# Kernel optimization log

Measured on AMD Instinct MI355X. Metric: run time of the kernel, lower is better.

The kernel has to match this reference:

```python
import jax, jax.numpy as jnp
import numpy as np

B, S, H, I, E, K = 2, 1024, 768, 1536, 8, 2
CAPACITY_FACTOR = 1.5
ROUTING_TEMP = 1.0
LB_WEIGHT = 0.001


def setup_inputs() -> dict:
    key = jax.random.key(0)
    k_x, k_g, k_w1, k_w3, k_w2 = jax.random.split(key, 5)
    std = 0.02
    return {
        "x": jax.random.normal(k_x, (B, S, H), dtype=jnp.float32),
        "w_gate": jax.random.normal(k_g, (H, E), dtype=jnp.float32) * 0.02,
        "w1": jax.random.normal(k_w1, (E, H, I), dtype=jnp.float32) * std,
        "w3": jax.random.normal(k_w3, (E, H, I), dtype=jnp.float32) * std,
        "w2": jax.random.normal(k_w2, (E, I, H), dtype=jnp.float32) * (std / np.sqrt(2 * 12)),
    }


def _moe_forward(x, w_gate, w1, w3, w2):
    Bb, Ss, Hh = x.shape
    T = Bb * Ss
    xf = x.reshape(T, Hh)

    # --- routing ---
    gate_logits = (xf @ w_gate) / ROUTING_TEMP          # [T, E]
    gate_probs = jax.nn.softmax(gate_logits, axis=-1)   # [T, E]
    topk_probs, topk_idx = jax.lax.top_k(gate_probs, K)  # [T, K]
    topk_probs = topk_probs / (topk_probs.sum(-1, keepdims=True) + 1e-8)

    # --- capacity dropping (per-k slot, token order, like the torch loop) ---
    capacity = max(8, int((T * K // E) * CAPACITY_FACTOR))
    onehot = (topk_idx[:, :, None] == jnp.arange(E)[None, None, :])  # [T, K, E] bool
    ranks = jnp.cumsum(onehot.astype(jnp.int32), axis=0)             # position of token in expert queue
    keep = onehot & (ranks <= capacity)                               # [T, K, E]

    # combine weight per (token, expert): sum over k of kept, clamped routing prob
    w_clamped = jnp.clip(topk_probs, 1e-8, 10.0)                      # [T, K]
    combine = jnp.einsum("tk,tke->te", w_clamped, keep.astype(xf.dtype))  # [T, E]

    # --- dense per-expert SwiGLU (reference form of masked dispatch) ---
    g = jnp.einsum("th,ehi->tei", xf, w1)   # [T, E, I]
    u = jnp.einsum("th,ehi->tei", xf, w3)   # [T, E, I]
    h = jax.nn.silu(g) * u                    # [T, E, I]
    y = jnp.einsum("tei,eih->teh", h, w2)   # [T, E, H]
    out = jnp.einsum("te,teh->th", combine, y).reshape(Bb, Ss, Hh)

    # --- load balancing loss ---
    expert_counts = keep.sum(axis=(0, 1)).astype(jnp.float32)         # [E]
    dropped = (onehot.sum() - keep.sum()).astype(jnp.float32)
    expert_usage = jax.lax.stop_gradient(expert_counts) / float(max(T * K, 1))
    gate_importance = gate_probs.mean(axis=0)                          # [E]
    aux = jnp.sum(expert_usage * gate_importance) * E
    aux = aux + jnp.where(dropped > 0, dropped / float(max(T, 1)) * 0.1, 0.0)
    aux = jnp.minimum(aux, 1.0) * LB_WEIGHT
    return out, aux


def reference(x, w_gate, w1, w3, w2):
    return _moe_forward(x, w_gate, w1, w3, w2)
```

## Files before the change

kernel.cpp:

```cpp
#include <hip/hip_runtime.h>
#include <math.h>

#define T_TOK 2048
#define HD 768
#define ID 1536
#define NE 8
#define CAP 768
#define TK 4096
#define RT 12
#define NB1 24
#define KC1 24
#define NB2 12
#define KC2 48
#define W2BLK 576

typedef __bf16 bf16_t;
typedef __bf16 bf16x8 __attribute__((ext_vector_type(8)));
typedef __bf16 bf16x4 __attribute__((ext_vector_type(4)));
typedef float floatx4 __attribute__((ext_vector_type(4)));

__device__ __forceinline__ void gld16(const bf16_t* g, bf16_t* l) {
  __builtin_amdgcn_global_load_lds(
      (__attribute__((address_space(1))) void*)(g),
      (__attribute__((address_space(3))) void*)(l),
      16, 0, 0);
}

__device__ __forceinline__ void repack_unit256(const float* __restrict__ src,
                                               bf16_t* __restrict__ dst, int C,
                                               int kc0, int tid) {
  int n = tid >> 2, p4 = tid & 3;
  int c8 = p4 ^ ((n >> 1) & 3);
  const float* sp0 = src + n + (size_t)(kc0 * 32 + c8 * 8) * C;
  bf16_t* dp = dst + (size_t)kc0 * 2048 + tid * 8;
#pragma unroll 2
  for (int t = 0; t < 8; ++t) {
    const float* sp = sp0 + (size_t)t * 32 * C;
    float v[8];
#pragma unroll
    for (int j = 0; j < 8; ++j) v[j] = sp[(size_t)j * C];
    bf16x8 o;
#pragma unroll
    for (int j = 0; j < 8; ++j) o[j] = (bf16_t)v[j];
    *(bf16x8*)(dp + t * 2048) = o;
  }
}

__device__ __forceinline__ void repack_unit1024(const float* __restrict__ src,
                                                bf16_t* __restrict__ dst, int C,
                                                int kc0, int tid1024) {
  int tid = tid1024 & 255;
  int tq = tid1024 >> 8;
  int n = tid >> 2, p4 = tid & 3;
  int c8 = p4 ^ ((n >> 1) & 3);
  const float* sp0 = src + n + (size_t)(kc0 * 32 + c8 * 8) * C;
  bf16_t* dp = dst + (size_t)kc0 * 2048 + tid * 8;
#pragma unroll
  for (int tt = 0; tt < 2; ++tt) {
    int t = tq * 2 + tt;
    const float* sp = sp0 + (size_t)t * 32 * C;
    float v[8];
#pragma unroll
    for (int j = 0; j < 8; ++j) v[j] = sp[(size_t)j * C];
    bf16x8 o;
#pragma unroll
    for (int j = 0; j < 8; ++j) o[j] = (bf16_t)v[j];
    *(bf16x8*)(dp + t * 2048) = o;
  }
}

__global__ void k_route(const float* __restrict__ x, const float* __restrict__ wg,
                        bf16_t* __restrict__ xbf, int2* __restrict__ idx2,
                        float2* __restrict__ wc2, float* __restrict__ probs8) {
  int b = blockIdx.x;
  int tid = threadIdx.x;
  int t = b * 4 + (tid >> 6);
  int lane = tid & 63;
  const float* xr = x + (size_t)t * HD;
  int off = lane * 12;
  float4 a = *(const float4*)(xr + off);
  float4 bv = *(const float4*)(xr + off + 4);
  float4 c = *(const float4*)(xr + off + 8);
  float xv[12] = {a.x, a.y, a.z, a.w, bv.x, bv.y, bv.z, bv.w, c.x, c.y, c.z, c.w};
  bf16x4 s0, s1, s2;
#pragma unroll
  for (int j = 0; j < 4; ++j) { s0[j] = (bf16_t)xv[j]; s1[j] = (bf16_t)xv[4 + j]; s2[j] = (bf16_t)xv[8 + j]; }
  bf16_t* xo = xbf + (size_t)t * HD + off;
  *(bf16x4*)xo = s0; *(bf16x4*)(xo + 4) = s1; *(bf16x4*)(xo + 8) = s2;

  float acc[8] = {0, 0, 0, 0, 0, 0, 0, 0};
#pragma unroll
  for (int jj = 0; jj < 12; ++jj) {
    const float4* wr = (const float4*)(wg + (size_t)(off + jj) * 8);
    float4 w0 = wr[0], w1v = wr[1];
    float v = xv[jj];
    acc[0] += v * w0.x; acc[1] += v * w0.y; acc[2] += v * w0.z; acc[3] += v * w0.w;
    acc[4] += v * w1v.x; acc[5] += v * w1v.y; acc[6] += v * w1v.z; acc[7] += v * w1v.w;
  }
#pragma unroll
  for (int e = 0; e < 8; ++e) {
    float v = acc[e];
    for (int s = 1; s < 64; s <<= 1) v += __shfl_xor(v, s, 64);
    acc[e] = v;
  }
  float mx = acc[0];
#pragma unroll
  for (int e = 1; e < 8; ++e) mx = fmaxf(mx, acc[e]);
  float p[8], sum = 0.f;
#pragma unroll
  for (int e = 0; e < 8; ++e) { p[e] = __expf(acc[e] - mx); sum += p[e]; }
#pragma unroll
  for (int e = 0; e < 8; ++e) p[e] /= sum;
  if (lane == 0) {
    float4 P0 = make_float4(p[0], p[1], p[2], p[3]);
    float4 P1 = make_float4(p[4], p[5], p[6], p[7]);
    *(float4*)&probs8[t * 8] = P0;
    *(float4*)&probs8[t * 8 + 4] = P1;
    int e0 = 0;
#pragma unroll
    for (int e = 1; e < 8; ++e) if (p[e] > p[e0]) e0 = e;
    int e1 = (e0 == 0) ? 1 : 0;
#pragma unroll
    for (int e = 0; e < 8; ++e) if (e != e0 && p[e] > p[e1]) e1 = e;
    float denom = p[e0] + p[e1] + 1e-8f;
    float w0c = fminf(fmaxf(p[e0] / denom, 1e-8f), 10.f);
    float w1c = fminf(fmaxf(p[e1] / denom, 1e-8f), 10.f);
    idx2[t] = make_int2(e0, e1);
    wc2[t] = make_float2(w0c, w1c);
  }
}

__global__ void k_scan(const int2* __restrict__ idx2, const float2* __restrict__ wc2,
                       const float* __restrict__ probs8,
                       const float* __restrict__ w1, const float* __restrict__ w3,
                       bf16_t* __restrict__ w1b, bf16_t* __restrict__ w3b,
                       int* __restrict__ tok_of_row, int2* __restrict__ rows2,
                       int2* __restrict__ cnt_start, float* __restrict__ aux_out) {
  if (blockIdx.x > 0) {
    int rb = blockIdx.x - 1;
    int m = rb >= 576;
    int r3 = m ? rb - 576 : rb;
    int pan = r3 / 3;
    int kc0 = (r3 - pan * 3) * 8;
    int e = pan & 7, nb = pan >> 3;
    const float* src = (m ? w3 : w1) + (size_t)e * HD * ID + nb * 64;
    bf16_t* dst = (m ? w3b : w1b) + (size_t)(e * NB1 + nb) * (KC1 * 2048);
    repack_unit1024(src, dst, ID, kc0, threadIdx.x);
    return;
  }
  __shared__ int2 sIdx[2048];
  __shared__ int sTot[16];
  __shared__ int sPos[8];
  __shared__ float sImp[16][8];
  int tid = threadIdx.x;
  sIdx[tid] = idx2[tid]; sIdx[tid + 1024] = idx2[tid + 1024];
  rows2[tid] = make_int2(-1, -1); rows2[tid + 1024] = make_int2(-1, -1);
  const float4* pp = (const float4*)probs8;
  float4 u0 = pp[tid * 4], u1 = pp[tid * 4 + 1], u2 = pp[tid * 4 + 2], u3 = pp[tid * 4 + 3];
  float im[8] = {u0.x + u2.x, u0.y + u2.y, u0.z + u2.z, u0.w + u2.w,
                 u1.x + u3.x, u1.y + u3.y, u1.z + u3.z, u1.w + u3.w};
#pragma unroll
  for (int e = 0; e < 8; ++e) {
    float v = im[e];
    for (int d = 1; d < 64; d <<= 1) v += __shfl_xor(v, d, 64);
    im[e] = v;
  }
  int w = tid >> 6, lane = tid & 63;
  if (lane == 0) {
#pragma unroll
    for (int e = 0; e < 8; ++e) sImp[w][e] = im[e];
  }
  __syncthreads();
  int s = w >> 3, e = w & 7;
  int t0 = lane * 32;
  int cnt = 0;
  for (int j = 0; j < 32; ++j) {
    int2 p = sIdx[t0 + j];
    cnt += ((s ? p.y : p.x) == e) ? 1 : 0;
  }
  int incl = cnt;
  for (int d = 1; d < 64; d <<= 1) {
    int v = __shfl_up(incl, d, 64);
    if (lane >= d) incl += v;
  }
  int excl = incl - cnt;
  if (lane == 63) sTot[w] = incl;
  __syncthreads();
  if (tid == 0) {
    int run = 0; float a = 0.f;
    for (int ee = 0; ee < 8; ++ee) {
      float impv = 0.f;
      for (int ww = 0; ww < 16; ++ww) impv += sImp[ww][ee];
      int k = min(sTot[ee], CAP) + min(sTot[8 + ee], CAP);
      sPos[ee] = run;
      cnt_start[ee] = make_int2(run, k);
      a += ((float)k / (float)TK) * (impv / (float)T_TOK);
      run += k;
    }
    a *= (float)NE;
    int dropped = TK - run;
    if (dropped > 0) a += (float)dropped / (float)T_TOK * 0.1f;
    aux_out[0] = fminf(a, 1.f) * 0.001f;
  }
  __syncthreads();
  int rank = excl;
  for (int j = 0; j < 32; ++j) {
    int t = t0 + j;
    int2 p = sIdx[t];
    int ex = s ? p.y : p.x;
    if (ex == e) {
      rank++;
      if (rank <= CAP) {
        int pos = atomicAdd(&sPos[e], 1);
        tok_of_row[pos] = t;
        ((int*)rows2)[2 * t + s] = pos;
      }
    }
  }
}

__global__ __launch_bounds__(256, 4)
void k_gemm1(const bf16_t* __restrict__ xbf, const bf16_t* __restrict__ w1b,
             const bf16_t* __restrict__ w3b, const float* __restrict__ w2,
             bf16_t* __restrict__ w2b, const int* __restrict__ tok_of_row,
             const int2* __restrict__ cnt_start, bf16_t* __restrict__ h_ws) {
  if (blockIdx.x < W2BLK) {
    int q = blockIdx.x;
    int pan = q / 6;
    int kc0 = (q - pan * 6) * 8;
    int e = pan & 7, nb = pan >> 3;
    const float* src = w2 + (size_t)e * ID * HD + nb * 64;
    bf16_t* dst = w2b + (size_t)(e * NB2 + nb) * (KC2 * 2048);
    repack_unit256(src, dst, HD, kc0, threadIdx.x);
    return;
  }
  int bx = blockIdx.x - W2BLK;
  int e = bx & 7;
  int t = bx >> 3;
  int nb = t / RT, rt = t - nb * RT;
  int2 cs = cnt_start[e];
  int nrows = cs.y - rt * 128;
  if (nrows <= 0) return;
  if (nrows > 128) nrows = 128;
  int grow0 = cs.x + rt * 128;

  __shared__ __attribute__((aligned(16))) bf16_t Abuf[2][128 * 32];
  __shared__ __attribute__((aligned(16))) bf16_t B1buf[2][64 * 32];
  __shared__ __attribute__((aligned(16))) bf16_t B3buf[2][64 * 32];

  int tid = threadIdx.x;
  int lane = tid & 63, wv = tid >> 6;
  int wm = wv & 1, wn = wv >> 1;
  int lr = lane & 15, q = lane >> 4;
  int rdc = (q ^ ((lane >> 1) & 3)) * 8;
  int srow = lane >> 2;
  int gch = ((lane & 3) ^ ((lane >> 3) & 3)) * 8;

  int ra = wv * 32 + srow;
  int tokA0 = tok_of_row[grow0 + min(ra, nrows - 1)];
  int tokA1 = tok_of_row[grow0 + min(ra + 16, nrows - 1)];
  const bf16_t* gA0 = xbf + (size_t)tokA0 * HD + gch;
  const bf16_t* gA1 = xbf + (size_t)tokA1 * HD + gch;
  const bf16_t* p1 = w1b + (size_t)((e * NB1 + nb) * KC1) * 2048 + tid * 8;
  const bf16_t* p3 = w3b + (size_t)((e * NB1 + nb) * KC1) * 2048 + tid * 8;

  floatx4 accg[4][2] = {};
  floatx4 accu[4][2] = {};

  gld16(gA0, &Abuf[0][wv * 1024]); gld16(gA1, &Abuf[0][wv * 1024 + 512]);
  gld16(p1, &B1buf[0][wv * 512]); gld16(p3, &B3buf[0][wv * 512]);
  gA0 += 32; gA1 += 32; p1 += 2048; p3 += 2048;
  __syncthreads();

  for (int kk = 0; kk < KC1; ++kk) {
    int cur = kk & 1;
    if (kk + 1 < KC1) {
      int nxt = cur ^ 1;
      gld16(gA0, &Abuf[nxt][wv * 1024]); gld16(gA1, &Abuf[nxt][wv * 1024 + 512]);
      gld16(p1, &B1buf[nxt][wv * 512]); gld16(p3, &B3buf[nxt][wv * 512]);
      gA0 += 32; gA1 += 32; p1 += 2048; p3 += 2048;
    }
    bf16x8 af[4], b1f[2], b3f[2];
#pragma unroll
    for (int i = 0; i < 4; ++i) af[i] = *(const bf16x8*)&Abuf[cur][(wm * 64 + i * 16 + lr) * 32 + rdc];
#pragma unroll
    for (int i = 0; i < 2; ++i) b1f[i] = *(const bf16x8*)&B1buf[cur][(wn * 32 + i * 16 + lr) * 32 + rdc];
#pragma unroll
    for (int i = 0; i < 2; ++i) b3f[i] = *(const bf16x8*)&B3buf[cur][(wn * 32 + i * 16 + lr) * 32 + rdc];
#pragma unroll
    for (int i = 0; i < 4; ++i)
#pragma unroll
      for (int jj = 0; jj < 2; ++jj) {
        accg[i][jj] = __builtin_amdgcn_mfma_f32_16x16x32_bf16(af[i], b1f[jj], accg[i][jj], 0, 0, 0);
        accu[i][jj] = __builtin_amdgcn_mfma_f32_16x16x32_bf16(af[i], b3f[jj], accu[i][jj], 0, 0, 0);
      }
    if (kk + 1 < KC1) __syncthreads();
  }
#pragma unroll
  for (int i = 0; i < 4; ++i)
#pragma unroll
    for (int r = 0; r < 4; ++r) {
      int rl = wm * 64 + i * 16 + q * 4 + r;
      if (rl < nrows) {
        size_t rb = (size_t)(grow0 + rl) * ID + nb * 64 + wn * 32 + lr;
#pragma unroll
        for (int jj = 0; jj < 2; ++jj) {
          float gg = accg[i][jj][r], uu = accu[i][jj][r];
          float sg = gg / (1.f + __expf(-gg));
          h_ws[rb + jj * 16] = (bf16_t)(sg * uu);
        }
      }
    }
}

__global__ __launch_bounds__(256, 4)
void k_gemm2(const bf16_t* __restrict__ h_ws, const bf16_t* __restrict__ w2b,
             const int2* __restrict__ cnt_start, float* __restrict__ y) {
  int e = blockIdx.x & 7;
  int t = blockIdx.x >> 3;
  int nb = t / RT, rt = t - nb * RT;
  int2 cs = cnt_start[e];
  int nrows = cs.y - rt * 128;
  if (nrows <= 0) return;
  if (nrows > 128) nrows = 128;
  int grow0 = cs.x + rt * 128;

  __shared__ __attribute__((aligned(16))) bf16_t Abuf[2][128 * 32];
  __shared__ __attribute__((aligned(16))) bf16_t Bbuf[2][64 * 32];

  int tid = threadIdx.x;
  int lane = tid & 63, wv = tid >> 6;
  int wm = wv & 1, wn = wv >> 1;
  int lr = lane & 15, q = lane >> 4;
  int rdc = (q ^ ((lane >> 1) & 3)) * 8;
  int srow = lane >> 2;
  int gch = ((lane & 3) ^ ((lane >> 3) & 3)) * 8;

  int ra = wv * 32 + srow;
  const bf16_t* gA0 = h_ws + (size_t)(grow0 + min(ra, nrows - 1)) * ID + gch;
  const bf16_t* gA1 = h_ws + (size_t)(grow0 + min(ra + 16, nrows - 1)) * ID + gch;
  const bf16_t* pB = w2b + (size_t)((e * NB2 + nb) * KC2) * 2048 + tid * 8;

  floatx4 acc[4][2] = {};

  gld16(gA0, &Abuf[0][wv * 1024]); gld16(gA1, &Abuf[0][wv * 1024 + 512]);
  gld16(pB, &Bbuf[0][wv * 512]);
  gA0 += 32; gA1 += 32; pB += 2048;
  __syncthreads();

  for (int kk = 0; kk < KC2; ++kk) {
    int cur = kk & 1;
    if (kk + 1 < KC2) {
      int nxt = cur ^ 1;
      gld16(gA0, &Abuf[nxt][wv * 1024]); gld16(gA1, &Abuf[nxt][wv * 1024 + 512]);
      gld16(pB, &Bbuf[nxt][wv * 512]);
      gA0 += 32; gA1 += 32; pB += 2048;
    }
    bf16x8 af[4], bfr[2];
#pragma unroll
    for (int i = 0; i < 4; ++i) af[i] = *(const bf16x8*)&Abuf[cur][(wm * 64 + i * 16 + lr) * 32 + rdc];
#pragma unroll
    for (int i = 0; i < 2; ++i) bfr[i] = *(const bf16x8*)&Bbuf[cur][(wn * 32 + i * 16 + lr) * 32 + rdc];
#pragma unroll
    for (int i = 0; i < 4; ++i)
#pragma unroll
      for (int jj = 0; jj < 2; ++jj)
        acc[i][jj] = __builtin_amdgcn_mfma_f32_16x16x32_bf16(af[i], bfr[jj], acc[i][jj], 0, 0, 0);
    if (kk + 1 < KC2) __syncthreads();
  }
#pragma unroll
  for (int i = 0; i < 4; ++i)
#pragma unroll
    for (int r = 0; r < 4; ++r) {
      int rl = wm * 64 + i * 16 + q * 4 + r;
      if (rl < nrows) {
        size_t ob = (size_t)(grow0 + rl) * HD + nb * 64 + wn * 32 + lr;
#pragma unroll
        for (int jj = 0; jj < 2; ++jj)
          y[ob + jj * 16] = acc[i][jj][r];
      }
    }
}

__global__ void k_comb(const float* __restrict__ y, const int2* __restrict__ rows2,
                       const float2* __restrict__ wc2, float* __restrict__ out) {
  int tid = threadIdx.x;
  int t = blockIdx.x * 4 + (tid >> 6);
  int lane = tid & 63;
  int2 r = rows2[t];
  float2 w = wc2[t];
  int off = lane * 12;
  floatx4 o0 = {0.f, 0.f, 0.f, 0.f}, o1 = o0, o2 = o0;
  if (r.x >= 0) {
    const float* yr = y + (size_t)r.x * HD + off;
    floatx4 a = *(const floatx4*)(yr);
    floatx4 b = *(const floatx4*)(yr + 4);
    floatx4 c = *(const floatx4*)(yr + 8);
    o0 += w.x * a; o1 += w.x * b; o2 += w.x * c;
  }
  if (r.y >= 0) {
    const float* yr = y + (size_t)r.y * HD + off;
    floatx4 a = *(const floatx4*)(yr);
    floatx4 b = *(const floatx4*)(yr + 4);
    floatx4 c = *(const floatx4*)(yr + 8);
    o0 += w.y * a; o1 += w.y * b; o2 += w.y * c;
  }
  float* op = out + (size_t)t * HD + off;
  *(floatx4*)(op) = o0;
  *(floatx4*)(op + 4) = o1;
  *(floatx4*)(op + 8) = o2;
}

extern "C" void kernel_launch(void* const* d_in, const int* in_sizes, int n_in,
                              void* d_out, int out_size, void* d_ws, size_t ws_size,
                              hipStream_t stream) {
  const float* x  = (const float*)d_in[0];
  const float* wg = (const float*)d_in[1];
  const float* w1 = (const float*)d_in[2];
  const float* w3 = (const float*)d_in[3];
  const float* w2 = (const float*)d_in[4];
  float* out = (float*)d_out;

  char* ws = (char*)d_ws;
  bf16_t* xbf  = (bf16_t*)(ws + 0);
  bf16_t* w1b  = (bf16_t*)(ws + 3145728);
  bf16_t* w3b  = (bf16_t*)(ws + 22020096);
  bf16_t* w2b  = (bf16_t*)(ws + 40894464);
  bf16_t* h_ws = (bf16_t*)(ws + 59768832);
  float*  probs8     = (float*)(ws + 72351744);
  int2*   idx2       = (int2*)(ws + 72417280);
  float2* wc2        = (float2*)(ws + 72433664);
  int*    tok_of_row = (int*)(ws + 72450048);
  int2*   rows2      = (int2*)(ws + 72466432);
  int2*   cnt_start  = (int2*)(ws + 72482816);
  float*  y_ws = (float*)(ws + 3145728);

  float* aux_out = out + (size_t)T_TOK * HD;

  k_route<<<512, 256, 0, stream>>>(x, wg, xbf, idx2, wc2, probs8);
  k_scan<<<1 + 1152, 1024, 0, stream>>>(idx2, wc2, probs8, w1, w3, w1b, w3b,
                                        tok_of_row, rows2, cnt_start, aux_out);
  k_gemm1<<<W2BLK + 8 * NB1 * RT, 256, 0, stream>>>(xbf, w1b, w3b, w2, w2b,
                                                    tok_of_row, cnt_start, h_ws);
  k_gemm2<<<8 * NB2 * RT, 256, 0, stream>>>(h_ws, w2b, cnt_start, y_ws);
  k_comb<<<512, 256, 0, stream>>>(y_ws, rows2, wc2, out);
}
```

Measured before the change: 238.4 us.

## Deepen LDS pipelining in expert GEMMs to triple and quad buffering

Both expert GEMM kernels move from double-buffered to deeper multi-stage LDS pipelines, three stages for the gate/up GEMM and four for the down GEMM. They use explicit vmcnt waits with raw s_barrier instead of __syncthreads, so several tiles' global-to-LDS loads stay in flight. The aim is to hide global load latency behind MFMA work. The cost is more shared memory per block, which may lower occupancy under the launch bounds, and the hand-counted vmcnt values must match the exact number of outstanding loads.

```diff
diff --git a/kernel.cpp b/kernel.cpp
--- a/kernel.cpp
+++ b/kernel.cpp
@@ -244,9 +244,9 @@
   if (nrows > 128) nrows = 128;
   int grow0 = cs.x + rt * 128;
 
-  __shared__ __attribute__((aligned(16))) bf16_t Abuf[2][128 * 32];
-  __shared__ __attribute__((aligned(16))) bf16_t B1buf[2][64 * 32];
-  __shared__ __attribute__((aligned(16))) bf16_t B3buf[2][64 * 32];
+  __shared__ __attribute__((aligned(16))) bf16_t Abuf[3][128 * 32];
+  __shared__ __attribute__((aligned(16))) bf16_t B1buf[3][64 * 32];
+  __shared__ __attribute__((aligned(16))) bf16_t B3buf[3][64 * 32];
 
   int tid = threadIdx.x;
   int lane = tid & 63, wv = tid >> 6;
@@ -267,19 +267,24 @@
   floatx4 accg[4][2] = {};
   floatx4 accu[4][2] = {};
 
-  gld16(gA0, &Abuf[0][wv * 1024]); gld16(gA1, &Abuf[0][wv * 1024 + 512]);
-  gld16(p1, &B1buf[0][wv * 512]); gld16(p3, &B3buf[0][wv * 512]);
-  gA0 += 32; gA1 += 32; p1 += 2048; p3 += 2048;
-  __syncthreads();
+#define STAGE1(j)                                                        \
+  do {                                                                   \
+    int s_ = (j) % 3;                                                    \
+    gld16(gA0 + (size_t)(j) * 32, &Abuf[s_][wv * 1024]);                 \
+    gld16(gA1 + (size_t)(j) * 32, &Abuf[s_][wv * 1024 + 512]);           \
+    gld16(p1 + (size_t)(j) * 2048, &B1buf[s_][wv * 512]);                \
+    gld16(p3 + (size_t)(j) * 2048, &B3buf[s_][wv * 512]);                \
+  } while (0)
+
+  STAGE1(0);
+  STAGE1(1);
+  asm volatile("s_waitcnt vmcnt(4)" ::: "memory");
+  __builtin_amdgcn_s_barrier();
+  __builtin_amdgcn_sched_barrier(0);
 
   for (int kk = 0; kk < KC1; ++kk) {
-    int cur = kk & 1;
-    if (kk + 1 < KC1) {
-      int nxt = cur ^ 1;
-      gld16(gA0, &Abuf[nxt][wv * 1024]); gld16(gA1, &Abuf[nxt][wv * 1024 + 512]);
-      gld16(p1, &B1buf[nxt][wv * 512]); gld16(p3, &B3buf[nxt][wv * 512]);
-      gA0 += 32; gA1 += 32; p1 += 2048; p3 += 2048;
-    }
+    int cur = kk % 3;
+    if (kk + 2 < KC1) STAGE1(kk + 2);
     bf16x8 af[4], b1f[2], b3f[2];
 #pragma unroll
     for (int i = 0; i < 4; ++i) af[i] = *(const bf16x8*)&Abuf[cur][(wm * 64 + i * 16 + lr) * 32 + rdc];
@@ -294,8 +299,18 @@
         accg[i][jj] = __builtin_amdgcn_mfma_f32_16x16x32_bf16(af[i], b1f[jj], accg[i][jj], 0, 0, 0);
         accu[i][jj] = __builtin_amdgcn_mfma_f32_16x16x32_bf16(af[i], b3f[jj], accu[i][jj], 0, 0, 0);
       }
-    if (kk + 1 < KC1) __syncthreads();
-  }
+    __builtin_amdgcn_sched_barrier(0);
+    if (kk + 1 < KC1) {
+      if (kk + 2 < KC1) {
+        asm volatile("s_waitcnt vmcnt(4)" ::: "memory");
+      } else {
+        asm volatile("s_waitcnt vmcnt(0)" ::: "memory");
+      }
+      __builtin_amdgcn_s_barrier();
+      __builtin_amdgcn_sched_barrier(0);
+    }
+  }
+#undef STAGE1
 #pragma unroll
   for (int i = 0; i < 4; ++i)
 #pragma unroll
@@ -325,8 +340,8 @@
   if (nrows > 128) nrows = 128;
   int grow0 = cs.x + rt * 128;
 
-  __shared__ __attribute__((aligned(16))) bf16_t Abuf[2][128 * 32];
-  __shared__ __attribute__((aligned(16))) bf16_t Bbuf[2][64 * 32];
+  __shared__ __attribute__((aligned(16))) bf16_t Abuf[4][128 * 32];
+  __shared__ __attribute__((aligned(16))) bf16_t Bbuf[4][64 * 32];
 
   int tid = threadIdx.x;
   int lane = tid & 63, wv = tid >> 6;
@@ -343,19 +358,24 @@
 
   floatx4 acc[4][2] = {};
 
-  gld16(gA0, &Abuf[0][wv * 1024]); gld16(gA1, &Abuf[0][wv * 1024 + 512]);
-  gld16(pB, &Bbuf[0][wv * 512]);
-  gA0 += 32; gA1 += 32; pB += 2048;
-  __syncthreads();
+#define STAGE2(j)                                                        \
+  do {                                                                   \
+    int s_ = (j) & 3;                                                    \
+    gld16(gA0 + (size_t)(j) * 32, &Abuf[s_][wv * 1024]);                 \
+    gld16(gA1 + (size_t)(j) * 32, &Abuf[s_][wv * 1024 + 512]);           \
+    gld16(pB + (size_t)(j) * 2048, &Bbuf[s_][wv * 512]);                 \
+  } while (0)
+
+  STAGE2(0);
+  STAGE2(1);
+  STAGE2(2);
+  asm volatile("s_waitcnt vmcnt(6)" ::: "memory");
+  __builtin_amdgcn_s_barrier();
+  __builtin_amdgcn_sched_barrier(0);
 
   for (int kk = 0; kk < KC2; ++kk) {
-    int cur = kk & 1;
-    if (kk + 1 < KC2) {
-      int nxt = cur ^ 1;
-      gld16(gA0, &Abuf[nxt][wv * 1024]); gld16(gA1, &Abuf[nxt][wv * 1024 + 512]);
-      gld16(pB, &Bbuf[nxt][wv * 512]);
-      gA0 += 32; gA1 += 32; pB += 2048;
-    }
+    int cur = kk & 3;
+    if (kk + 3 < KC2) STAGE2(kk + 3);
     bf16x8 af[4], bfr[2];
 #pragma unroll
     for (int i = 0; i < 4; ++i) af[i] = *(const bf16x8*)&Abuf[cur][(wm * 64 + i * 16 + lr) * 32 + rdc];
@@ -366,8 +386,20 @@
 #pragma unroll
       for (int jj = 0; jj < 2; ++jj)
         acc[i][jj] = __builtin_amdgcn_mfma_f32_16x16x32_bf16(af[i], bfr[jj], acc[i][jj], 0, 0, 0);
-    if (kk + 1 < KC2) __syncthreads();
-  }
+    __builtin_amdgcn_sched_barrier(0);
+    if (kk + 1 < KC2) {
+      if (kk + 3 < KC2) {
+        asm volatile("s_waitcnt vmcnt(6)" ::: "memory");
+      } else if (kk + 2 < KC2) {
+        asm volatile("s_waitcnt vmcnt(3)" ::: "memory");
+      } else {
+        asm volatile("s_waitcnt vmcnt(0)" ::: "memory");
+      }
+      __builtin_amdgcn_s_barrier();
+      __builtin_amdgcn_sched_barrier(0);
+    }
+  }
+#undef STAGE2
 #pragma unroll
   for (int i = 0; i < 4; ++i)
 #pragma unroll
```

Result: slower. 248.0 us (+4.0%).

## Widen gemm1 N tile to 128 and drop LDS double buffering

Applied to the files above, without the earlier changes.

The gate/up GEMM tile grows from 128x64 to 128x128 output columns per block, so each block reuses its gathered A rows across twice as many columns and the grid halves. The LDS buffers become single-buffered, with a sync before and after each load stage, and occupancy hints drop to 2 blocks per CU to make room for the doubled accumulators. This cuts redundant A-gather traffic, but load latency is no longer overlapped with MFMA work inside a block and fewer blocks are resident.

```diff
diff --git a/kernel.cpp b/kernel.cpp
--- a/kernel.cpp
+++ b/kernel.cpp
@@ -9,6 +9,7 @@
 #define TK 4096
 #define RT 12
 #define NB1 24
+#define NB1X 12
 #define KC1 24
 #define NB2 12
 #define KC2 48
@@ -219,7 +220,7 @@
   }
 }
 
-__global__ __launch_bounds__(256, 4)
+__global__ __launch_bounds__(256, 2)
 void k_gemm1(const bf16_t* __restrict__ xbf, const bf16_t* __restrict__ w1b,
              const bf16_t* __restrict__ w3b, const float* __restrict__ w2,
              bf16_t* __restrict__ w2b, const int* __restrict__ tok_of_row,
@@ -244,9 +245,9 @@
   if (nrows > 128) nrows = 128;
   int grow0 = cs.x + rt * 128;
 
-  __shared__ __attribute__((aligned(16))) bf16_t Abuf[2][128 * 32];
-  __shared__ __attribute__((aligned(16))) bf16_t B1buf[2][64 * 32];
-  __shared__ __attribute__((aligned(16))) bf16_t B3buf[2][64 * 32];
+  __shared__ __attribute__((aligned(16))) bf16_t Abuf[128 * 32];
+  __shared__ __attribute__((aligned(16))) bf16_t B1buf[128 * 32];
+  __shared__ __attribute__((aligned(16))) bf16_t B3buf[128 * 32];
 
   int tid = threadIdx.x;
   int lane = tid & 63, wv = tid >> 6;
@@ -261,40 +262,39 @@
   int tokA1 = tok_of_row[grow0 + min(ra + 16, nrows - 1)];
   const bf16_t* gA0 = xbf + (size_t)tokA0 * HD + gch;
   const bf16_t* gA1 = xbf + (size_t)tokA1 * HD + gch;
-  const bf16_t* p1 = w1b + (size_t)((e * NB1 + nb) * KC1) * 2048 + tid * 8;
-  const bf16_t* p3 = w3b + (size_t)((e * NB1 + nb) * KC1) * 2048 + tid * 8;
-
-  floatx4 accg[4][2] = {};
-  floatx4 accu[4][2] = {};
-
-  gld16(gA0, &Abuf[0][wv * 1024]); gld16(gA1, &Abuf[0][wv * 1024 + 512]);
-  gld16(p1, &B1buf[0][wv * 512]); gld16(p3, &B3buf[0][wv * 512]);
-  gA0 += 32; gA1 += 32; p1 += 2048; p3 += 2048;
-  __syncthreads();
+  const bf16_t* p1 = w1b + (size_t)((e * NB1 + nb * 2 + (wv >> 1)) * KC1) * 2048 +
+                     (wv & 1) * 1024 + lane * 8;
+  const bf16_t* p3 = w3b + (size_t)((e * NB1 + nb * 2 + (wv >> 1)) * KC1) * 2048 +
+                     (wv & 1) * 1024 + lane * 8;
+  bf16_t* lA0 = &Abuf[(wv * 32) * 32];
+  bf16_t* lA1 = &Abuf[(wv * 32 + 16) * 32];
+  bf16_t* lB1 = &B1buf[wv * 1024];
+  bf16_t* lB3 = &B3buf[wv * 1024];
+
+  floatx4 accg[4][4] = {};
+  floatx4 accu[4][4] = {};
 
   for (int kk = 0; kk < KC1; ++kk) {
-    int cur = kk & 1;
-    if (kk + 1 < KC1) {
-      int nxt = cur ^ 1;
-      gld16(gA0, &Abuf[nxt][wv * 1024]); gld16(gA1, &Abuf[nxt][wv * 1024 + 512]);
-      gld16(p1, &B1buf[nxt][wv * 512]); gld16(p3, &B3buf[nxt][wv * 512]);
-      gA0 += 32; gA1 += 32; p1 += 2048; p3 += 2048;
-    }
-    bf16x8 af[4], b1f[2], b3f[2];
-#pragma unroll
-    for (int i = 0; i < 4; ++i) af[i] = *(const bf16x8*)&Abuf[cur][(wm * 64 + i * 16 + lr) * 32 + rdc];
-#pragma unroll
-    for (int i = 0; i < 2; ++i) b1f[i] = *(const bf16x8*)&B1buf[cur][(wn * 32 + i * 16 + lr) * 32 + rdc];
-#pragma unroll
-    for (int i = 0; i < 2; ++i) b3f[i] = *(const bf16x8*)&B3buf[cur][(wn * 32 + i * 16 + lr) * 32 + rdc];
+    __syncthreads();
+    gld16(gA0, lA0); gld16(gA1, lA1);
+    gld16(p1, lB1); gld16(p1 + 512, lB1 + 512);
+    gld16(p3, lB3); gld16(p3 + 512, lB3 + 512);
+    gA0 += 32; gA1 += 32; p1 += 2048; p3 += 2048;
+    __syncthreads();
+    bf16x8 af[4], b1f[4], b3f[4];
+#pragma unroll
+    for (int i = 0; i < 4; ++i) af[i] = *(const bf16x8*)&Abuf[(wm * 64 + i * 16 + lr) * 32 + rdc];
+#pragma unroll
+    for (int i = 0; i < 4; ++i) b1f[i] = *(const bf16x8*)&B1buf[wn * 2048 + (i * 16 + lr) * 32 + rdc];
+#pragma unroll
+    for (int i = 0; i < 4; ++i) b3f[i] = *(const bf16x8*)&B3buf[wn * 2048 + (i * 16 + lr) * 32 + rdc];
 #pragma unroll
     for (int i = 0; i < 4; ++i)
 #pragma unroll
-      for (int jj = 0; jj < 2; ++jj) {
+      for (int jj = 0; jj < 4; ++jj) {
         accg[i][jj] = __builtin_amdgcn_mfma_f32_16x16x32_bf16(af[i], b1f[jj], accg[i][jj], 0, 0, 0);
         accu[i][jj] = __builtin_amdgcn_mfma_f32_16x16x32_bf16(af[i], b3f[jj], accu[i][jj], 0, 0, 0);
       }
-    if (kk + 1 < KC1) __syncthreads();
   }
 #pragma unroll
   for (int i = 0; i < 4; ++i)
@@ -302,9 +302,9 @@
     for (int r = 0; r < 4; ++r) {
       int rl = wm * 64 + i * 16 + q * 4 + r;
       if (rl < nrows) {
-        size_t rb = (size_t)(grow0 + rl) * ID + nb * 64 + wn * 32 + lr;
-#pragma unroll
-        for (int jj = 0; jj < 2; ++jj) {
+        size_t rb = (size_t)(grow0 + rl) * ID + nb * 128 + wn * 64 + lr;
+#pragma unroll
+        for (int jj = 0; jj < 4; ++jj) {
           float gg = accg[i][jj][r], uu = accu[i][jj][r];
           float sg = gg / (1.f + __expf(-gg));
           h_ws[rb + jj * 16] = (bf16_t)(sg * uu);
@@ -440,8 +440,8 @@
   k_route<<<512, 256, 0, stream>>>(x, wg, xbf, idx2, wc2, probs8);
   k_scan<<<1 + 1152, 1024, 0, stream>>>(idx2, wc2, probs8, w1, w3, w1b, w3b,
                                         tok_of_row, rows2, cnt_start, aux_out);
-  k_gemm1<<<W2BLK + 8 * NB1 * RT, 256, 0, stream>>>(xbf, w1b, w3b, w2, w2b,
-                                                    tok_of_row, cnt_start, h_ws);
+  k_gemm1<<<W2BLK + 8 * NB1X * RT, 256, 0, stream>>>(xbf, w1b, w3b, w2, w2b,
+                                                     tok_of_row, cnt_start, h_ws);
   k_gemm2<<<8 * NB2 * RT, 256, 0, stream>>>(h_ws, w2b, cnt_start, y_ws);
   k_comb<<<512, 256, 0, stream>>>(y_ws, rows2, wc2, out);
 }
```

Measured after the change: 245.7 us. 1.03x slower.
